# Performance work log

Measured on AMD Instinct MI355X. Metric: run time of the kernel, lower is better.

## Reference

```python
import jax, jax.numpy as jnp
import numpy as np

V, NJ, NSHAPE, NEXP, B = 5023, 5, 100, 50, 1024
PARENTS = np.array([-1, 0, 1, 1, 1])  # FLAME kinematic tree: global, neck, jaw, eyeL, eyeR


def rodrigues(rot_vecs):
    """Axis-angle [..., 3] -> rotation matrices [..., 3, 3] (SMPL-style, eps-safe)."""
    angle = jnp.linalg.norm(rot_vecs + 1e-8, axis=-1, keepdims=True)  # [...,1]
    axis = rot_vecs / angle
    cos = jnp.cos(angle)[..., None]
    sin = jnp.sin(angle)[..., None]
    rx, ry, rz = axis[..., 0], axis[..., 1], axis[..., 2]
    z = jnp.zeros_like(rx)
    K = jnp.stack([z, -rz, ry, rz, z, -rx, -ry, rx, z], axis=-1).reshape(rot_vecs.shape[:-1] + (3, 3))
    eye = jnp.eye(3, dtype=rot_vecs.dtype)
    return eye + sin * K + (1.0 - cos) * (K @ K)


def setup_inputs() -> dict:
    ks = jax.random.split(jax.random.key(0), 8)
    shape_params = jax.random.normal(ks[0], (B, NSHAPE), jnp.float32)
    expression_params = jax.random.normal(ks[1], (B, NEXP), jnp.float32)
    pose_params = 0.1 * jax.random.normal(ks[2], (B, 6), jnp.float32)
    v_template = jax.random.normal(ks[3], (V, 3), jnp.float32)
    shapedirs = 0.01 * jax.random.normal(ks[4], (V, 3, NSHAPE + NEXP), jnp.float32)
    posedirs = 0.01 * jax.random.normal(ks[5], ((NJ - 1) * 9, V * 3), jnp.float32)
    jr = jax.random.uniform(ks[6], (NJ, V), jnp.float32)
    J_regressor = jr / jr.sum(axis=1, keepdims=True)
    w = jax.random.uniform(ks[7], (V, NJ), jnp.float32)
    lbs_weights = w / w.sum(axis=1, keepdims=True)
    return dict(shape_params=shape_params, expression_params=expression_params,
                pose_params=pose_params, v_template=v_template, shapedirs=shapedirs,
                posedirs=posedirs, J_regressor=J_regressor, lbs_weights=lbs_weights)


def reference(shape_params, expression_params, pose_params, v_template,
              shapedirs, posedirs, J_regressor, lbs_weights):
    b = shape_params.shape[0]
    dt = shape_params.dtype
    # full_pose = [global(3), neck(3)=0, jaw(3), eyes(6)=0]
    zeros3 = jnp.zeros((b, 3), dt)
    zeros6 = jnp.zeros((b, 6), dt)
    full_pose = jnp.concatenate([pose_params[:, :3], zeros3, pose_params[:, 3:], zeros6], axis=1)
    betas = jnp.concatenate([shape_params, expression_params], axis=1)  # [b, 150]

    # shape blendshapes
    v_shaped = v_template[None] + jnp.einsum('bl,vcl->bvc', betas, shapedirs)  # [b,V,3]
    joints = jnp.einsum('jv,bvc->bjc', J_regressor, v_shaped)                 # [b,J,3]

    # pose blendshapes
    rot_mats = rodrigues(full_pose.reshape(b, NJ, 3))                         # [b,J,3,3]
    eye3 = jnp.eye(3, dtype=dt)
    pose_feature = (rot_mats[:, 1:] - eye3).reshape(b, (NJ - 1) * 9)
    v_posed = v_shaped + (pose_feature @ posedirs).reshape(b, V, 3)

    # rigid kinematic chain
    rel_joints = joints.at[:, 1:].add(-joints[:, PARENTS[1:]])                # [b,J,3]
    bottom = jnp.broadcast_to(jnp.array([0.0, 0.0, 0.0, 1.0], dt), (b, NJ, 1, 4))
    tmats = jnp.concatenate([jnp.concatenate([rot_mats, rel_joints[..., None]], axis=-1), bottom], axis=-2)  # [b,J,4,4]
    chain = [tmats[:, 0]]
    for i in range(1, NJ):  # fixed 5-joint tree
        chain.append(chain[PARENTS[i]] @ tmats[:, i])
    transforms = jnp.stack(chain, axis=1)                                     # [b,J,4,4]
    joints_h = jnp.concatenate([joints, jnp.zeros((b, NJ, 1), dt)], axis=-1)[..., None]  # [b,J,4,1]
    rel_transforms = transforms - jnp.pad(transforms @ joints_h, ((0, 0), (0, 0), (0, 0), (3, 0)))  # [b,J,4,4]

    # linear blend skinning
    T = jnp.einsum('vj,bjxy->bvxy', lbs_weights, rel_transforms)              # [b,V,4,4]
    v_h = jnp.concatenate([v_posed, jnp.ones((b, V, 1), dt)], axis=-1)        # [b,V,4]
    vertices = jnp.einsum('bvxy,bvy->bvx', T, v_h)[..., :3]                   # [b,V,3]
    return vertices, T
```

## Files before the change

kernel.cpp:

```cpp
#include <hip/hip_runtime.h>
#include <hip/hip_bf16.h>

#define VN     5023
#define NBATCH 1024
#define N3     15069
#define NPAD   15168
#define KS     5
#define NKG    20

typedef short bf16x8 __attribute__((ext_vector_type(8)));
typedef float f32x4  __attribute__((ext_vector_type(4)));

__device__ __forceinline__ short f2bf(float x) {
    __hip_bfloat16 h = __float2bfloat16(x);
    return *reinterpret_cast<short*>(&h);
}

__global__ void k0_bf(const float* __restrict__ sd, const float* __restrict__ vt,
                      bf16x8* __restrict__ sdpB) {
    int i = blockIdx.x * 256 + threadIdx.x;
    if (i >= NKG * NPAD) return;
    int kg = i / NPAD, n = i - kg * NPAD;
    int kbase = (kg >> 2) * 32 + (kg & 3) * 8;
    bf16x8 out;
#pragma unroll
    for (int e = 0; e < 8; e++) {
        int k = kbase + e;
        float val = 0.f;
        if (n < N3) {
            if (k < 150)       val = sd[(size_t)n * 150 + k];
            else if (k == 150) val = vt[n];
        }
        out[e] = f2bf(val);
    }
    sdpB[i] = out;
}

__global__ void k1_js(const float* __restrict__ jr, const float* __restrict__ sd,
                      const float* __restrict__ vt, float* __restrict__ JS) {
    int j3c = blockIdx.x;
    int j = j3c / 3, c = j3c - 3 * j;
    int l = threadIdx.x;
    if (l >= 152) return;
    int v0 = blockIdx.y * 157, v1 = min(v0 + 157, VN);
    float acc = 0.0f;
    for (int v = v0; v < v1; ++v) {
        float w = jr[j * VN + v];
        float s = (l < 150) ? sd[(size_t)(v * 3 + c) * 150 + l]
                            : ((l == 150) ? vt[v * 3 + c] : 0.f);
        acc += w * s;
    }
    atomicAdd(&JS[j3c * 152 + l], acc);
}

__device__ __forceinline__ void rodrigues3(float x, float y, float z, float* R) {
    float ax = x + 1e-8f, ay = y + 1e-8f, az = z + 1e-8f;
    float ang = sqrtf(ax * ax + ay * ay + az * az);
    float inv = 1.0f / ang;
    float ux = x * inv, uy = y * inv, uz = z * inv;
    float co = cosf(ang), si = sinf(ang), t1 = 1.0f - co;
    float K[9] = {0.f, -uz, uy,  uz, 0.f, -ux,  -uy, ux, 0.f};
    float K2[9];
#pragma unroll
    for (int r = 0; r < 3; r++)
#pragma unroll
        for (int cc = 0; cc < 3; cc++) {
            float a = 0.f;
#pragma unroll
            for (int k = 0; k < 3; k++) a += K[r * 3 + k] * K[k * 3 + cc];
            K2[r * 3 + cc] = a;
        }
#pragma unroll
    for (int i = 0; i < 9; i++) {
        float e = (i == 0 || i == 4 || i == 8) ? 1.f : 0.f;
        R[i] = e + si * K[i] + t1 * K2[i];
    }
}

__global__ void k2_pose(const float* __restrict__ shp, const float* __restrict__ expr,
                        const float* __restrict__ pose, const float* __restrict__ JS,
                        bf16x8* __restrict__ betasA, float* __restrict__ pf9,
                        float* __restrict__ rel) {
    int b = blockIdx.x;
    int tt = threadIdx.x;
    __shared__ float sB[152];
    __shared__ float sJ[15];
    for (int l = tt; l < 152; l += 64) {
        float val = 0.0f;
        if (l < 100) val = shp[b * 100 + l];
        else if (l < 150) val = expr[b * 50 + (l - 100)];
        else if (l == 150) val = 1.0f;
        sB[l] = val;
    }
    __syncthreads();
    for (int l = tt; l < 160; l += 64) {
        float val = (l < 152) ? sB[l] : 0.f;
        int kg = (l >> 5) * 4 + ((l >> 3) & 3);
        short* dst = (short*)betasA;
        dst[((size_t)kg * NBATCH + b) * 8 + (l & 7)] = f2bf(val);
    }
    if (tt < 15) {
        float acc = 0.0f;
        const float* row = JS + tt * 152;
        for (int l = 0; l < 152; ++l) acc += row[l] * sB[l];
        sJ[tt] = acc;
    }
    __syncthreads();
    if (tt == 0) {
        float p[6];
#pragma unroll
        for (int i = 0; i < 6; i++) p[i] = pose[b * 6 + i];
        float R0[9], RJ[9];
        rodrigues3(p[0], p[1], p[2], R0);
        rodrigues3(p[3], p[4], p[5], RJ);
        float Jm[5][3];
#pragma unroll
        for (int jj = 0; jj < 5; jj++)
#pragma unroll
            for (int cc = 0; cc < 3; cc++) Jm[jj][cc] = sJ[jj * 3 + cc];
        float rj[5][3];
#pragma unroll
        for (int cc = 0; cc < 3; cc++) {
            rj[0][cc] = Jm[0][cc];
            rj[1][cc] = Jm[1][cc] - Jm[0][cc];
            rj[2][cc] = Jm[2][cc] - Jm[1][cc];
            rj[3][cc] = Jm[3][cc] - Jm[1][cc];
            rj[4][cc] = Jm[4][cc] - Jm[1][cc];
        }
        float tw[5][3];
#pragma unroll
        for (int cc = 0; cc < 3; cc++) tw[0][cc] = rj[0][cc];
#pragma unroll
        for (int cc = 0; cc < 3; cc++)
            tw[1][cc] = R0[cc * 3 + 0] * rj[1][0] + R0[cc * 3 + 1] * rj[1][1] + R0[cc * 3 + 2] * rj[1][2] + tw[0][cc];
#pragma unroll
        for (int jj = 2; jj < 5; jj++)
#pragma unroll
            for (int cc = 0; cc < 3; cc++)
                tw[jj][cc] = R0[cc * 3 + 0] * rj[jj][0] + R0[cc * 3 + 1] * rj[jj][1] + R0[cc * 3 + 2] * rj[jj][2] + tw[1][cc];
        float R2w[9];
#pragma unroll
        for (int r = 0; r < 3; r++)
#pragma unroll
            for (int cc = 0; cc < 3; cc++) {
                float a = 0.f;
#pragma unroll
                for (int k = 0; k < 3; k++) a += R0[r * 3 + k] * RJ[k * 3 + cc];
                R2w[r * 3 + cc] = a;
            }
        float* ro = rel + b * 80;
#pragma unroll
        for (int jj = 0; jj < 5; jj++) {
            const float* Rw = (jj == 2) ? R2w : R0;
#pragma unroll
            for (int rr = 0; rr < 3; rr++) {
                ro[jj * 16 + rr * 4 + 0] = Rw[rr * 3 + 0];
                ro[jj * 16 + rr * 4 + 1] = Rw[rr * 3 + 1];
                ro[jj * 16 + rr * 4 + 2] = Rw[rr * 3 + 2];
                float tj = Rw[rr * 3 + 0] * Jm[jj][0] + Rw[rr * 3 + 1] * Jm[jj][1] + Rw[rr * 3 + 2] * Jm[jj][2];
                ro[jj * 16 + rr * 4 + 3] = tw[jj][rr] - tj;
            }
            ro[jj * 16 + 12] = 0.f; ro[jj * 16 + 13] = 0.f; ro[jj * 16 + 14] = 0.f; ro[jj * 16 + 15] = 1.f;
        }
        float* pf = pf9 + b * 12;
#pragma unroll
        for (int e = 0; e < 9; e++) pf[e] = RJ[e] - ((e == 0 || e == 4 || e == 8) ? 1.f : 0.f);
        pf[9] = 0.f; pf[10] = 0.f; pf[11] = 0.f;
    }
}

__global__ void __launch_bounds__(256, 2)
k3_mfma(const bf16x8* __restrict__ sdpB, const bf16x8* __restrict__ betasA,
        const float* __restrict__ pd, const float* __restrict__ lw,
        const float* __restrict__ pf9, const float* __restrict__ rel,
        float* __restrict__ outv, float* __restrict__ outT) {
    __shared__ float vsh[16][200];

    int tid = threadIdx.x;
    int w = tid >> 6, l = tid & 63;
    int row16 = l & 15, g = l >> 4;
    int b0 = blockIdx.y * 16;
    int n0 = blockIdx.x * 192;

    bf16x8 afr[5];
#pragma unroll
    for (int ks = 0; ks < 5; ks++)
        afr[ks] = betasA[(size_t)(ks * 4 + g) * NBATCH + b0 + row16];

    f32x4 acc0 = {0.f, 0.f, 0.f, 0.f}, acc1 = acc0, acc2 = acc0;
    {
        int ntb = n0 + (w * 3) * 16 + row16;
#pragma unroll
        for (int ks = 0; ks < 5; ks++) {
            size_t base = (size_t)(ks * 4 + g) * NPAD;
            acc0 = __builtin_amdgcn_mfma_f32_16x16x32_bf16(afr[ks], sdpB[base + ntb],      acc0, 0, 0, 0);
            acc1 = __builtin_amdgcn_mfma_f32_16x16x32_bf16(afr[ks], sdpB[base + ntb + 16], acc1, 0, 0, 0);
            acc2 = __builtin_amdgcn_mfma_f32_16x16x32_bf16(afr[ks], sdpB[base + ntb + 32], acc2, 0, 0, 0);
        }
    }
    {
        int nl = (w * 3) * 16 + row16;
#pragma unroll
        for (int r = 0; r < 4; r++) {
            vsh[g * 4 + r][nl]      = acc0[r];
            vsh[g * 4 + r][nl + 16] = acc1[r];
            vsh[g * 4 + r][nl + 32] = acc2[r];
        }
    }

    int v_loc = tid & 63;
    int v = blockIdx.x * 64 + v_loc;
    bool vok = v < VN;
    int vc_ = vok ? v : VN - 1;
    float wj[5], pdv[9][3];
#pragma unroll
    for (int j = 0; j < 5; j++) wj[j] = lw[vc_ * 5 + j];
#pragma unroll
    for (int k = 0; k < 9; k++)
#pragma unroll
        for (int c = 0; c < 3; c++) pdv[k][c] = pd[(size_t)(9 + k) * N3 + vc_ * 3 + c];

    __syncthreads();

#pragma unroll
    for (int i = 0; i < 4; i++) {
        int bl = w * 4 + i;
        int b = b0 + bl;
        const float* pf = pf9 + b * 12;
        const float* rb = rel + b * 80;
        float vp[3];
#pragma unroll
        for (int c = 0; c < 3; c++) {
            float x = vsh[bl][v_loc * 3 + c];
#pragma unroll
            for (int k = 0; k < 9; k++) x += pf[k] * pdv[k][c];
            vp[c] = x;
        }
        float T[16];
#pragma unroll
        for (int e = 0; e < 16; e++) T[e] = 0.0f;
#pragma unroll
        for (int j = 0; j < 5; j++) {
            float wgt = wj[j];
            const float4 r0 = *(const float4*)(rb + j * 16 + 0);
            const float4 r1 = *(const float4*)(rb + j * 16 + 4);
            const float4 r2 = *(const float4*)(rb + j * 16 + 8);
            const float4 r3 = *(const float4*)(rb + j * 16 + 12);
            T[0]  += wgt * r0.x;  T[1]  += wgt * r0.y;  T[2]  += wgt * r0.z;  T[3]  += wgt * r0.w;
            T[4]  += wgt * r1.x;  T[5]  += wgt * r1.y;  T[6]  += wgt * r1.z;  T[7]  += wgt * r1.w;
            T[8]  += wgt * r2.x;  T[9]  += wgt * r2.y;  T[10] += wgt * r2.z;  T[11] += wgt * r2.w;
            T[12] += wgt * r3.x;  T[13] += wgt * r3.y;  T[14] += wgt * r3.z;  T[15] += wgt * r3.w;
        }
        float vo[3];
#pragma unroll
        for (int rr = 0; rr < 3; rr++)
            vo[rr] = T[rr * 4 + 0] * vp[0] + T[rr * 4 + 1] * vp[1] + T[rr * 4 + 2] * vp[2] + T[rr * 4 + 3];

        if (vok) {
            size_t vbase = (size_t)b * VN + v;
            float* pv = outv + vbase * 3;
            pv[0] = vo[0]; pv[1] = vo[1]; pv[2] = vo[2];
            float4* pT = (float4*)(outT + vbase * 16);
            pT[0] = make_float4(T[0],  T[1],  T[2],  T[3]);
            pT[1] = make_float4(T[4],  T[5],  T[6],  T[7]);
            pT[2] = make_float4(T[8],  T[9],  T[10], T[11]);
            pT[3] = make_float4(T[12], T[13], T[14], T[15]);
        }
    }
}

extern "C" void kernel_launch(void* const* d_in, const int* in_sizes, int n_in,
                              void* d_out, int out_size, void* d_ws, size_t ws_size,
                              hipStream_t stream) {
    const float* shp  = (const float*)d_in[0];
    const float* expr = (const float*)d_in[1];
    const float* pose = (const float*)d_in[2];
    const float* vt   = (const float*)d_in[3];
    const float* sd   = (const float*)d_in[4];
    const float* pd   = (const float*)d_in[5];
    const float* jr   = (const float*)d_in[6];
    const float* lw   = (const float*)d_in[7];

    float* outv = (float*)d_out;
    float* outT = outv + (size_t)NBATCH * VN * 3;

    char* w = (char*)d_ws;
    const size_t SDPB_B  = (size_t)NKG * NPAD * 16;
    const size_t BETA_B  = (size_t)NKG * NBATCH * 16;
    const size_t JS_B    = 15 * 152 * 4;
    const size_t PF9_B   = (size_t)NBATCH * 12 * 4;
    bf16x8* sdpB   = (bf16x8*)w;
    bf16x8* betasA = (bf16x8*)(w + SDPB_B);
    float*  JS     = (float*)(w + SDPB_B + BETA_B);
    float*  pf9    = (float*)(w + SDPB_B + BETA_B + JS_B);
    float*  rel    = (float*)(w + SDPB_B + BETA_B + JS_B + PF9_B);

    hipMemsetAsync(JS, 0, JS_B, stream);
    k0_bf<<<(NKG * NPAD + 255) / 256, 256, 0, stream>>>(sd, vt, sdpB);
    k1_js<<<dim3(15, 32), 192, 0, stream>>>(jr, sd, vt, JS);
    k2_pose<<<NBATCH, 64, 0, stream>>>(shp, expr, pose, JS, betasA, pf9, rel);
    k3_mfma<<<dim3(NPAD / 192, NBATCH / 16), 256, 0, stream>>>(sdpB, betasA, pd, lw, pf9, rel, outv, outT);
}
```

Baseline: 269.1 us.

## Split fused MFMA+skinning kernel into posed-vertex and LBS kernels

```diff
diff --git a/kernel.cpp b/kernel.cpp
--- a/kernel.cpp
+++ b/kernel.cpp
@@ -5,7 +5,6 @@
 #define NBATCH 1024
 #define N3     15069
 #define NPAD   15168
-#define KS     5
 #define NKG    20
 
 typedef short bf16x8 __attribute__((ext_vector_type(8)));
@@ -170,10 +169,9 @@
 }
 
 __global__ void __launch_bounds__(256, 2)
-k3_mfma(const bf16x8* __restrict__ sdpB, const bf16x8* __restrict__ betasA,
-        const float* __restrict__ pd, const float* __restrict__ lw,
-        const float* __restrict__ pf9, const float* __restrict__ rel,
-        float* __restrict__ outv, float* __restrict__ outT) {
+k3_vp(const bf16x8* __restrict__ sdpB, const bf16x8* __restrict__ betasA,
+      const float* __restrict__ pd, const float* __restrict__ pf9,
+      float* __restrict__ vposed) {
     __shared__ float vsh[16][200];
 
     int tid = threadIdx.x;
@@ -212,9 +210,7 @@
     int v = blockIdx.x * 64 + v_loc;
     bool vok = v < VN;
     int vc_ = vok ? v : VN - 1;
-    float wj[5], pdv[9][3];
-#pragma unroll
-    for (int j = 0; j < 5; j++) wj[j] = lw[vc_ * 5 + j];
+    float pdv[9][3];
 #pragma unroll
     for (int k = 0; k < 9; k++)
 #pragma unroll
@@ -227,7 +223,6 @@
         int bl = w * 4 + i;
         int b = b0 + bl;
         const float* pf = pf9 + b * 12;
-        const float* rb = rel + b * 80;
         float vp[3];
 #pragma unroll
         for (int c = 0; c < 3; c++) {
@@ -236,37 +231,42 @@
             for (int k = 0; k < 9; k++) x += pf[k] * pdv[k][c];
             vp[c] = x;
         }
-        float T[16];
-#pragma unroll
-        for (int e = 0; e < 16; e++) T[e] = 0.0f;
-#pragma unroll
-        for (int j = 0; j < 5; j++) {
-            float wgt = wj[j];
-            const float4 r0 = *(const float4*)(rb + j * 16 + 0);
-            const float4 r1 = *(const float4*)(rb + j * 16 + 4);
-            const float4 r2 = *(const float4*)(rb + j * 16 + 8);
-            const float4 r3 = *(const float4*)(rb + j * 16 + 12);
-            T[0]  += wgt * r0.x;  T[1]  += wgt * r0.y;  T[2]  += wgt * r0.z;  T[3]  += wgt * r0.w;
-            T[4]  += wgt * r1.x;  T[5]  += wgt * r1.y;  T[6]  += wgt * r1.z;  T[7]  += wgt * r1.w;
-            T[8]  += wgt * r2.x;  T[9]  += wgt * r2.y;  T[10] += wgt * r2.z;  T[11] += wgt * r2.w;
-            T[12] += wgt * r3.x;  T[13] += wgt * r3.y;  T[14] += wgt * r3.z;  T[15] += wgt * r3.w;
-        }
-        float vo[3];
-#pragma unroll
-        for (int rr = 0; rr < 3; rr++)
-            vo[rr] = T[rr * 4 + 0] * vp[0] + T[rr * 4 + 1] * vp[1] + T[rr * 4 + 2] * vp[2] + T[rr * 4 + 3];
-
         if (vok) {
-            size_t vbase = (size_t)b * VN + v;
-            float* pv = outv + vbase * 3;
-            pv[0] = vo[0]; pv[1] = vo[1]; pv[2] = vo[2];
-            float4* pT = (float4*)(outT + vbase * 16);
-            pT[0] = make_float4(T[0],  T[1],  T[2],  T[3]);
-            pT[1] = make_float4(T[4],  T[5],  T[6],  T[7]);
-            pT[2] = make_float4(T[8],  T[9],  T[10], T[11]);
-            pT[3] = make_float4(T[12], T[13], T[14], T[15]);
-        }
-    }
+            float* pv = vposed + ((size_t)b * VN + v) * 3;
+            pv[0] = vp[0]; pv[1] = vp[1]; pv[2] = vp[2];
+        }
+    }
+}
+
+__global__ void __launch_bounds__(256, 8)
+k4_lbs(const float* __restrict__ lw, const float* __restrict__ rel,
+       float* __restrict__ outv, float* __restrict__ outT) {
+    int b = blockIdx.y;
+    int v = blockIdx.x * 256 + threadIdx.x;
+    if (v >= VN) return;
+    const float* rb = rel + b * 80;
+
+    size_t vbase = (size_t)b * VN + v;
+    float* pv = outv + vbase * 3;
+    float vp0 = pv[0], vp1 = pv[1], vp2 = pv[2];
+    float w0 = lw[v * 5 + 0], w1 = lw[v * 5 + 1], w2 = lw[v * 5 + 2];
+    float w3 = lw[v * 5 + 3], w4 = lw[v * 5 + 4];
+
+    float T[16];
+#pragma unroll
+    for (int e = 0; e < 16; e++)
+        T[e] = w0 * rb[e] + w1 * rb[16 + e] + w2 * rb[32 + e] + w3 * rb[48 + e] + w4 * rb[64 + e];
+
+    float vo0 = T[0]  * vp0 + T[1]  * vp1 + T[2]  * vp2 + T[3];
+    float vo1 = T[4]  * vp0 + T[5]  * vp1 + T[6]  * vp2 + T[7];
+    float vo2 = T[8]  * vp0 + T[9]  * vp1 + T[10] * vp2 + T[11];
+
+    pv[0] = vo0; pv[1] = vo1; pv[2] = vo2;
+    float4* pT = (float4*)(outT + vbase * 16);
+    pT[0] = make_float4(T[0],  T[1],  T[2],  T[3]);
+    pT[1] = make_float4(T[4],  T[5],  T[6],  T[7]);
+    pT[2] = make_float4(T[8],  T[9],  T[10], T[11]);
+    pT[3] = make_float4(T[12], T[13], T[14], T[15]);
 }
 
 extern "C" void kernel_launch(void* const* d_in, const int* in_sizes, int n_in,
@@ -285,10 +285,10 @@
     float* outT = outv + (size_t)NBATCH * VN * 3;
 
     char* w = (char*)d_ws;
-    const size_t SDPB_B  = (size_t)NKG * NPAD * 16;
-    const size_t BETA_B  = (size_t)NKG * NBATCH * 16;
-    const size_t JS_B    = 15 * 152 * 4;
-    const size_t PF9_B   = (size_t)NBATCH * 12 * 4;
+    const size_t SDPB_B = (size_t)NKG * NPAD * 16;
+    const size_t BETA_B = (size_t)NKG * NBATCH * 16;
+    const size_t JS_B   = 15 * 152 * 4;
+    const size_t PF9_B  = (size_t)NBATCH * 12 * 4;
     bf16x8* sdpB   = (bf16x8*)w;
     bf16x8* betasA = (bf16x8*)(w + SDPB_B);
     float*  JS     = (float*)(w + SDPB_B + BETA_B);
@@ -299,5 +299,6 @@
     k0_bf<<<(NKG * NPAD + 255) / 256, 256, 0, stream>>>(sd, vt, sdpB);
     k1_js<<<dim3(15, 32), 192, 0, stream>>>(jr, sd, vt, JS);
     k2_pose<<<NBATCH, 64, 0, stream>>>(shp, expr, pose, JS, betasA, pf9, rel);
-    k3_mfma<<<dim3(NPAD / 192, NBATCH / 16), 256, 0, stream>>>(sdpB, betasA, pd, lw, pf9, rel, outv, outT);
-}
+    k3_vp<<<dim3(NPAD / 192, NBATCH / 16), 256, 0, stream>>>(sdpB, betasA, pd, pf9, outv);
+    k4_lbs<<<dim3((VN + 255) / 256, NBATCH), 256, 0, stream>>>(lw, rel, outv, outT);
+}
```

New measurement: 255.8 us. -5.0%, faster.
